# Performance work log

Measured on AMD Instinct MI355X. Metric: run time of the kernel, lower is better.

The kernel has to match this reference:

```python
import jax, jax.numpy as jnp
import numpy as np


def setup_inputs() -> dict:
    key = jax.random.key(0)
    ks = jax.random.split(key, 7)
    B, P, D = 4, 2048, 1024
    s = 1.0 / np.sqrt(D)
    return {
        "x":  jax.random.normal(ks[0], (B, P, D), dtype=jnp.float32),
        "Wq": jax.random.normal(ks[1], (D, D), dtype=jnp.float32) * s,
        "bq": jnp.zeros((D,), dtype=jnp.float32),
        "Wk": jax.random.normal(ks[2], (D, D), dtype=jnp.float32) * s,
        "bk": jnp.zeros((D,), dtype=jnp.float32),
        "Wv": jax.random.normal(ks[3], (D, D), dtype=jnp.float32) * s,
        "bv": jnp.zeros((D,), dtype=jnp.float32),
    }


def reference(x, Wq, bq, Wk, bk, Wv, bv):
    # x: [B, P, D]; Linear uses W stored torch-style [out, in]: y = x @ W.T + b
    b, p, d = x.shape
    q = jnp.einsum("bpd,ed->bpe", x, Wq) + bq
    k = jnp.einsum("bpd,ed->bpe", x, Wk) + bk
    v = jnp.einsum("bpd,ed->bpe", x, Wv) + bv
    attn = jnp.einsum("bqd,bkd->bqk", q, k)  # [B, P, P]
    causal = jnp.triu(jnp.ones((p, p), dtype=bool), k=1)  # True above diagonal
    attn = jnp.where(causal, -jnp.inf, attn)
    attn = attn / jnp.sqrt(jnp.asarray(d, dtype=attn.dtype))
    scores = jax.nn.softmax(attn, axis=-1)
    # dropout is identity in eval/deterministic mode
    return jnp.einsum("bqk,bkd->bqd", scores, v)
```

## Files before the change

### kernel.cpp

```cpp
#include <hip/hip_runtime.h>
#include <hip/hip_bf16.h>


typedef __attribute__((ext_vector_type(8))) short bf16x8;
typedef __attribute__((ext_vector_type(4))) float f32x4;

__device__ __forceinline__ unsigned short f2bf(float f) {
    union { float f; unsigned u; } v; v.f = f;
    unsigned r = v.u + 0x7FFF + ((v.u >> 16) & 1);
    return (unsigned short)(r >> 16);
}

__device__ __forceinline__ void gload_lds16(const unsigned short* g, unsigned short* l) {
    __builtin_amdgcn_global_load_lds(
        (const __attribute__((address_space(1))) unsigned int*)g,
        (__attribute__((address_space(3))) unsigned int*)l, 16, 0, 0);
}

__global__ void convert_kernel(const float* __restrict__ x,  const float* __restrict__ wq,
                               const float* __restrict__ wk, const float* __restrict__ wv,
                               const float* __restrict__ bq, const float* __restrict__ bk,
                               const float* __restrict__ bv,
                               unsigned short* __restrict__ xb, unsigned short* __restrict__ wqkvb,
                               float* __restrict__ bqkv, float* __restrict__ lsum) {
    long t = (long)blockIdx.x * blockDim.x + threadIdx.x;
    long idx = t * 4;
    const float* src; unsigned short* dst; long off;
    if      (idx <  8388608) { src = x;  dst = xb;            off = idx;            }
    else if (idx <  9437184) { src = wq; dst = wqkvb;         off = idx -  8388608; }
    else if (idx < 10485760) { src = wk; dst = wqkvb+1048576; off = idx -  9437184; }
    else if (idx < 11534336) { src = wv; dst = wqkvb+2097152; off = idx - 10485760; }
    else return;
    float4 v = *(const float4*)(src + off);
    ushort4 o = make_ushort4(f2bf(v.x), f2bf(v.y), f2bf(v.z), f2bf(v.w));
    *(ushort4*)(dst + off) = o;
    if (t < 768) {
        long o2 = t * 4;
        float4 b;
        if      (o2 < 1024) b = *(const float4*)(bq + o2);
        else if (o2 < 2048) b = *(const float4*)(bk + o2 - 1024);
        else                b = *(const float4*)(bv + o2 - 2048);
        *(float4*)(bqkv + o2) = b;
    }
    if (t >= 1024 && t < 3072) {
        float4 z = make_float4(0.f, 0.f, 0.f, 0.f);
        *(float4*)(lsum + (t - 1024) * 4) = z;
    }
}

__device__ __forceinline__ void stage(const unsigned short* gA, long lda,
                                      const unsigned short* gB, long ldb,
                                      unsigned short* As, unsigned short* Bs,
                                      int w, int k0) {
#pragma unroll
    for (int s = 0; s < 4; ++s) {
        gload_lds16(gA + k0 + (long)(s * 8) * lda, &As[(w * 32 + s * 8) * 64]);
        gload_lds16(gB + k0 + (long)(s * 8) * ldb, &Bs[(w * 32 + s * 8) * 64]);
    }
}

template<bool SWAP>
__device__ __forceinline__ void mfma_tile(const unsigned short* As, const unsigned short* Bs,
                                          int wr, int wc, int ln, int pr0, int pr1,
                                          f32x4 (&acc)[4][4]) {
#pragma unroll
    for (int kk = 0; kk < 2; ++kk) {
        const int pr = kk ? pr1 : pr0;
        bf16x8 af[4], bfr[4];
#pragma unroll
        for (int i = 0; i < 4; ++i)
            af[i] = *(const bf16x8*)(&As[(wr + i * 16 + ln) * 64 + pr]);
#pragma unroll
        for (int j = 0; j < 4; ++j)
            bfr[j] = *(const bf16x8*)(&Bs[(wc + j * 16 + ln) * 64 + pr]);
#pragma unroll
        for (int i = 0; i < 4; ++i)
#pragma unroll
            for (int j = 0; j < 4; ++j)
                acc[i][j] = SWAP
                    ? __builtin_amdgcn_mfma_f32_16x16x32_bf16(bfr[j], af[i], acc[i][j], 0, 0, 0)
                    : __builtin_amdgcn_mfma_f32_16x16x32_bf16(af[i], bfr[j], acc[i][j], 0, 0, 0);
    }
}

template<bool SWAP>
__device__ __forceinline__ void kloop_sb(const unsigned short* gA, long lda,
                                         const unsigned short* gB, long ldb,
                                         unsigned short* As, unsigned short* Bs,
                                         int w, int lane, int Keff, f32x4 (&acc)[4][4]) {
    const int q  = lane >> 4;
    const int ln = lane & 15;
    const int wr = (w >> 1) * 64;
    const int wc = (w & 1) * 64;
    const int pr0 = ((q)     ^ (ln & 7)) * 8;
    const int pr1 = ((q + 4) ^ (ln & 7)) * 8;
    for (int k0 = 0; k0 < Keff; k0 += 64) {
        stage(gA, lda, gB, ldb, As, Bs, w, k0);
        __syncthreads();
        mfma_tile<SWAP>(As, Bs, wr, wc, ln, pr0, pr1, acc);
        __syncthreads();
    }
}

template<bool SWAP>
__device__ __forceinline__ void kloop_db(const unsigned short* gA, long lda,
                                         const unsigned short* gB, long ldb,
                                         unsigned short* As0, unsigned short* Bs0,
                                         unsigned short* As1, unsigned short* Bs1,
                                         int w, int lane, int Keff, f32x4 (&acc)[4][4]) {
    const int q  = lane >> 4;
    const int ln = lane & 15;
    const int wr = (w >> 1) * 64;
    const int wc = (w & 1) * 64;
    const int pr0 = ((q)     ^ (ln & 7)) * 8;
    const int pr1 = ((q + 4) ^ (ln & 7)) * 8;
    stage(gA, lda, gB, ldb, As0, Bs0, w, 0);
    __syncthreads();
    for (int k0 = 0; k0 < Keff; k0 += 128) {
        stage(gA, lda, gB, ldb, As1, Bs1, w, k0 + 64);
        mfma_tile<SWAP>(As0, Bs0, wr, wc, ln, pr0, pr1, acc);
        __syncthreads();
        if (k0 + 128 < Keff)
            stage(gA, lda, gB, ldb, As0, Bs0, w, k0 + 128);
        mfma_tile<SWAP>(As1, Bs1, wr, wc, ln, pr0, pr1, acc);
        __syncthreads();
    }
}

__global__ __launch_bounds__(256, 3)
void gemm_qkv(const unsigned short* __restrict__ X,
              const unsigned short* __restrict__ W,
              unsigned short* __restrict__ QK,
              unsigned short* __restrict__ VT,
              const float* __restrict__ bias) {
    const int n0 = blockIdx.x * 128;
    const int m0 = blockIdx.y * 128;
    __shared__ __align__(16) unsigned short As0[128 * 64];
    __shared__ __align__(16) unsigned short Bs0[128 * 64 + 8192];
    const int tid = threadIdx.x, lane = tid & 63, w = tid >> 6;
    const int q = lane >> 4, ln = lane & 15;
    const int wr = (w >> 1) * 64, wc = (w & 1) * 64;
    const int srow = lane >> 3, sc = (lane & 7) ^ srow;
    const unsigned short* gA = X + (long)(m0 + w * 32 + srow) * 1024 + sc * 8;
    const unsigned short* gB = W + (long)(n0 + w * 32 + srow) * 1024 + sc * 8;
    f32x4 acc[4][4] = {};
    if (n0 >= 2048) {
        kloop_sb<false>(gA, 1024, gB, 1024, As0, Bs0, w, lane, 1024, acc);
#pragma unroll
        for (int j = 0; j < 4; ++j) {
            const int e = n0 - 2048 + wc + j * 16 + ln;
            const float bc = bias[n0 + wc + j * 16 + ln];
#pragma unroll
            for (int i = 0; i < 4; ++i) {
                const int m = m0 + wr + i * 16 + q * 4;
                ushort4 o = make_ushort4(f2bf(acc[i][j][0] + bc), f2bf(acc[i][j][1] + bc),
                                         f2bf(acc[i][j][2] + bc), f2bf(acc[i][j][3] + bc));
                *(ushort4*)(VT + (long)e * 8192 + m) = o;
            }
        }
    } else {
        kloop_sb<true>(gA, 1024, gB, 1024, As0, Bs0, w, lane, 1024, acc);
#pragma unroll
        for (int j = 0; j < 4; ++j) {
            const float4 bc = *(const float4*)(bias + n0 + wc + j * 16 + q * 4);
#pragma unroll
            for (int i = 0; i < 4; ++i) {
                const int m = m0 + wr + i * 16 + ln;
                const int n = n0 + wc + j * 16 + q * 4;
                ushort4 o = make_ushort4(f2bf(acc[i][j][0] + bc.x), f2bf(acc[i][j][1] + bc.y),
                                         f2bf(acc[i][j][2] + bc.z), f2bf(acc[i][j][3] + bc.w));
                *(ushort4*)(QK + (long)m * 2048 + n) = o;
            }
        }
    }
}

__device__ __forceinline__ void stage64(const unsigned short* gA, const unsigned short* gB,
                                        unsigned short* As, unsigned short* Bs,
                                        int w, int k0) {
    gload_lds16(gA + k0,                     &As[(w * 8) * 64]);
    gload_lds16(gA + k0 + (long)32 * 2048,   &As[(32 + w * 8) * 64]);
#pragma unroll
    for (int s = 0; s < 4; ++s)
        gload_lds16(gB + k0 + (long)(s * 32) * 2048, &Bs[(s * 32 + w * 8) * 64]);
}

__device__ __forceinline__ void mfma_tile64(const unsigned short* As, const unsigned short* Bs,
                                            int wr, int wc, int ln, int pr0, int pr1,
                                            f32x4 (&acc)[2][4]) {
#pragma unroll
    for (int kk = 0; kk < 2; ++kk) {
        const int pr = kk ? pr1 : pr0;
        bf16x8 af[2], bfr[4];
#pragma unroll
        for (int i = 0; i < 2; ++i)
            af[i] = *(const bf16x8*)(&As[(wr + i * 16 + ln) * 64 + pr]);
#pragma unroll
        for (int j = 0; j < 4; ++j)
            bfr[j] = *(const bf16x8*)(&Bs[(wc + j * 16 + ln) * 64 + pr]);
#pragma unroll
        for (int i = 0; i < 2; ++i)
#pragma unroll
            for (int j = 0; j < 4; ++j)
                acc[i][j] = __builtin_amdgcn_mfma_f32_16x16x32_bf16(bfr[j], af[i], acc[i][j], 0, 0, 0);
    }
}

__global__ __launch_bounds__(256, 3)
void gemm_scores(const unsigned short* __restrict__ QK,
                 unsigned short* __restrict__ P,
                 float* __restrict__ lsum) {
    const int t = blockIdx.x;
    int g = (int)((sqrtf(4.0f * t + 1.0f) - 1.0f) * 0.5f);
    while ((g + 1) * (g + 2) <= t) ++g;
    while (g * (g + 1) > t) --g;
    const int r  = t - g * (g + 1);
    const int gp = g + 1;
    const int i64 = 2 * g + (r >= gp ? 1 : 0);
    const int j   = (r >= gp) ? (r - gp) : r;
    const int m0 = i64 * 64, n0 = j * 128, z = blockIdx.y;
    const unsigned short* Qz = QK + (long)z * 2048 * 2048;
    const unsigned short* Kz = Qz + 1024;
    unsigned short* Pz = P + (long)z * 2048 * 2048;
    float* lz = lsum + z * 2048;

    __shared__ __align__(16) unsigned short As0[64 * 64], Bs0[128 * 64];
    __shared__ __align__(16) unsigned short As1[64 * 64], Bs1[128 * 64];
    const int tid = threadIdx.x, lane = tid & 63, w = tid >> 6;
    const int q = lane >> 4, ln = lane & 15;
    const int wr = (w >> 1) * 32, wc = (w & 1) * 64;
    const int srow = lane >> 3, sc = (lane & 7) ^ srow;
    const int pr0 = ((q)     ^ (ln & 7)) * 8;
    const int pr1 = ((q + 4) ^ (ln & 7)) * 8;
    const unsigned short* gA = Qz + (long)(m0 + w * 8 + srow) * 2048 + sc * 8;
    const unsigned short* gB = Kz + (long)(n0 + w * 8 + srow) * 2048 + sc * 8;
    f32x4 acc[2][4] = {};

    stage64(gA, gB, As0, Bs0, w, 0);
    __syncthreads();
    for (int k0 = 0; k0 < 1024; k0 += 128) {
        stage64(gA, gB, As1, Bs1, w, k0 + 64);
        mfma_tile64(As0, Bs0, wr, wc, ln, pr0, pr1, acc);
        __syncthreads();
        if (k0 + 128 < 1024)
            stage64(gA, gB, As0, Bs0, w, k0 + 128);
        mfma_tile64(As1, Bs1, wr, wc, ln, pr0, pr1, acc);
        __syncthreads();
    }

    const float scale = 0.03125f;
#pragma unroll
    for (int i2 = 0; i2 < 2; ++i2) {
        const int m = m0 + wr + i2 * 16 + ln;
        float rs = 0.f;
#pragma unroll
        for (int j2 = 0; j2 < 4; ++j2) {
            const int n = n0 + wc + j2 * 16 + q * 4;
            float p0 = (n     <= m) ? __expf(acc[i2][j2][0] * scale) : 0.f;
            float p1 = (n + 1 <= m) ? __expf(acc[i2][j2][1] * scale) : 0.f;
            float p2 = (n + 2 <= m) ? __expf(acc[i2][j2][2] * scale) : 0.f;
            float p3 = (n + 3 <= m) ? __expf(acc[i2][j2][3] * scale) : 0.f;
            rs += (p0 + p1) + (p2 + p3);
            ushort4 o = make_ushort4(f2bf(p0), f2bf(p1), f2bf(p2), f2bf(p3));
            *(ushort4*)(Pz + (long)m * 2048 + n) = o;
        }
        rs += __shfl_xor(rs, 16); rs += __shfl_xor(rs, 32);
        if (lane < 16) atomicAdd(&lz[m], rs);
    }
}

__global__ __launch_bounds__(256, 2)
void gemm_pv(const unsigned short* __restrict__ P,
             const unsigned short* __restrict__ VT,
             const float* __restrict__ lsum,
             float* __restrict__ out) {
    const int L  = blockIdx.x;
    const int ph = L >> 8;
    const int c  = L & 255;
    const int z  = c >> 6;
    const int r  = c & 63;
    const int mh = r >> 3;
    const int nt = r & 7;
    const int mt = ph ? 15 - mh : mh;
    const int m0 = mt * 128, n0 = nt * 128;
    const int Keff = m0 + 128;
    const unsigned short* Pz = P + (long)z * 2048 * 2048;
    const unsigned short* Vz = VT + (long)z * 2048;
    const float* lz = lsum + z * 2048;

    __shared__ __align__(16) unsigned short As0[128 * 64], Bs0[128 * 64];
    __shared__ __align__(16) unsigned short As1[128 * 64], Bs1[128 * 64];
    const int tid = threadIdx.x, lane = tid & 63, w = tid >> 6;
    const int q = lane >> 4, ln = lane & 15;
    const int wr = (w >> 1) * 64, wc = (w & 1) * 64;
    const int srow = lane >> 3, sc = (lane & 7) ^ srow;
    const unsigned short* gA = Pz + (long)(m0 + w * 32 + srow) * 2048 + sc * 8;
    const unsigned short* gB = Vz + (long)(n0 + w * 32 + srow) * 8192 + sc * 8;
    f32x4 acc[4][4] = {};
    kloop_db<true>(gA, 2048, gB, 8192, As0, Bs0, As1, Bs1, w, lane, Keff, acc);

#pragma unroll
    for (int i2 = 0; i2 < 4; ++i2) {
        const int m = m0 + wr + i2 * 16 + ln;
        const float inv = 1.0f / lz[m];
#pragma unroll
        for (int j2 = 0; j2 < 4; ++j2) {
            const int n = n0 + wc + j2 * 16 + q * 4;
            f32x4 o;
            o[0] = acc[i2][j2][0] * inv; o[1] = acc[i2][j2][1] * inv;
            o[2] = acc[i2][j2][2] * inv; o[3] = acc[i2][j2][3] * inv;
            __builtin_nontemporal_store(o, (f32x4*)(out + (long)(z * 2048 + m) * 1024 + n));
        }
    }
}

extern "C" void kernel_launch(void* const* d_in, const int* in_sizes, int n_in,
                              void* d_out, int out_size, void* d_ws, size_t ws_size,
                              hipStream_t stream) {
    const float* x  = (const float*)d_in[0];
    const float* Wq = (const float*)d_in[1];
    const float* bq = (const float*)d_in[2];
    const float* Wk = (const float*)d_in[3];
    const float* bk = (const float*)d_in[4];
    const float* Wv = (const float*)d_in[5];
    const float* bv = (const float*)d_in[6];
    float* out = (float*)d_out;

    char* ws = (char*)d_ws;
    unsigned short* xb    = (unsigned short*)ws; ws += (long)8192 * 1024 * 2;
    unsigned short* wqkvb = (unsigned short*)ws; ws += (long)3072 * 1024 * 2;
    float*          bqkv  = (float*)ws;          ws += (long)3072 * 4;
    float*          lsum  = (float*)ws;          ws += (long)8192 * 4;
    unsigned short* QKb   = (unsigned short*)ws; ws += (long)8192 * 2048 * 2;
    unsigned short* VTb   = (unsigned short*)ws; ws += (long)1024 * 8192 * 2;
    unsigned short* Pb    = (unsigned short*)ws; ws += (long)4 * 2048 * 2048 * 2;

    hipLaunchKernelGGL(convert_kernel, dim3(11264), dim3(256), 0, stream,
                       x, Wq, Wk, Wv, bq, bk, bv, xb, wqkvb, bqkv, lsum);

    hipLaunchKernelGGL(gemm_qkv, dim3(24, 64, 1), dim3(256), 0, stream,
                       xb, wqkvb, QKb, VTb, bqkv);

    hipLaunchKernelGGL(gemm_scores, dim3(272, 4, 1), dim3(256), 0, stream,
                       QKb, Pb, lsum);

    hipLaunchKernelGGL(gemm_pv, dim3(512, 1, 1), dim3(256), 0, stream,
                       Pb, VTb, lsum, out);
}
```

Before: 232.2 us.

## Use 64-row tiles with longest-first scheduling in PV GEMM

```diff
diff --git a/kernel.cpp b/kernel.cpp
--- a/kernel.cpp
+++ b/kernel.cpp
@@ -102,31 +102,6 @@
     }
 }
 
-template<bool SWAP>
-__device__ __forceinline__ void kloop_db(const unsigned short* gA, long lda,
-                                         const unsigned short* gB, long ldb,
-                                         unsigned short* As0, unsigned short* Bs0,
-                                         unsigned short* As1, unsigned short* Bs1,
-                                         int w, int lane, int Keff, f32x4 (&acc)[4][4]) {
-    const int q  = lane >> 4;
-    const int ln = lane & 15;
-    const int wr = (w >> 1) * 64;
-    const int wc = (w & 1) * 64;
-    const int pr0 = ((q)     ^ (ln & 7)) * 8;
-    const int pr1 = ((q + 4) ^ (ln & 7)) * 8;
-    stage(gA, lda, gB, ldb, As0, Bs0, w, 0);
-    __syncthreads();
-    for (int k0 = 0; k0 < Keff; k0 += 128) {
-        stage(gA, lda, gB, ldb, As1, Bs1, w, k0 + 64);
-        mfma_tile<SWAP>(As0, Bs0, wr, wc, ln, pr0, pr1, acc);
-        __syncthreads();
-        if (k0 + 128 < Keff)
-            stage(gA, lda, gB, ldb, As0, Bs0, w, k0 + 128);
-        mfma_tile<SWAP>(As1, Bs1, wr, wc, ln, pr0, pr1, acc);
-        __syncthreads();
-    }
-}
-
 __global__ __launch_bounds__(256, 3)
 void gemm_qkv(const unsigned short* __restrict__ X,
               const unsigned short* __restrict__ W,
@@ -175,14 +150,15 @@
     }
 }
 
-__device__ __forceinline__ void stage64(const unsigned short* gA, const unsigned short* gB,
+__device__ __forceinline__ void stage64(const unsigned short* gA, long lda,
+                                        const unsigned short* gB, long ldb,
                                         unsigned short* As, unsigned short* Bs,
                                         int w, int k0) {
-    gload_lds16(gA + k0,                     &As[(w * 8) * 64]);
-    gload_lds16(gA + k0 + (long)32 * 2048,   &As[(32 + w * 8) * 64]);
+    gload_lds16(gA + k0,                  &As[(w * 8) * 64]);
+    gload_lds16(gA + k0 + (long)32 * lda, &As[(32 + w * 8) * 64]);
 #pragma unroll
     for (int s = 0; s < 4; ++s)
-        gload_lds16(gB + k0 + (long)(s * 32) * 2048, &Bs[(s * 32 + w * 8) * 64]);
+        gload_lds16(gB + k0 + (long)(s * 32) * ldb, &Bs[(s * 32 + w * 8) * 64]);
 }
 
 __device__ __forceinline__ void mfma_tile64(const unsigned short* As, const unsigned short* Bs,
@@ -236,14 +212,14 @@
     const unsigned short* gB = Kz + (long)(n0 + w * 8 + srow) * 2048 + sc * 8;
     f32x4 acc[2][4] = {};
 
-    stage64(gA, gB, As0, Bs0, w, 0);
+    stage64(gA, 2048, gB, 2048, As0, Bs0, w, 0);
     __syncthreads();
     for (int k0 = 0; k0 < 1024; k0 += 128) {
-        stage64(gA, gB, As1, Bs1, w, k0 + 64);
+        stage64(gA, 2048, gB, 2048, As1, Bs1, w, k0 + 64);
         mfma_tile64(As0, Bs0, wr, wc, ln, pr0, pr1, acc);
         __syncthreads();
         if (k0 + 128 < 1024)
-            stage64(gA, gB, As0, Bs0, w, k0 + 128);
+            stage64(gA, 2048, gB, 2048, As0, Bs0, w, k0 + 128);
         mfma_tile64(As1, Bs1, wr, wc, ln, pr0, pr1, acc);
         __syncthreads();
     }
@@ -269,38 +245,48 @@
     }
 }
 
-__global__ __launch_bounds__(256, 2)
+__global__ __launch_bounds__(256, 3)
 void gemm_pv(const unsigned short* __restrict__ P,
              const unsigned short* __restrict__ VT,
              const float* __restrict__ lsum,
              float* __restrict__ out) {
-    const int L  = blockIdx.x;
-    const int ph = L >> 8;
-    const int c  = L & 255;
-    const int z  = c >> 6;
-    const int r  = c & 63;
-    const int mh = r >> 3;
-    const int nt = r & 7;
-    const int mt = ph ? 15 - mh : mh;
-    const int m0 = mt * 128, n0 = nt * 128;
-    const int Keff = m0 + 128;
+    const int L   = blockIdx.x;
+    const int z   = L & 3;
+    const int r   = L >> 2;
+    const int i64 = 31 - (r >> 3);
+    const int nt  = r & 7;
+    const int m0  = i64 * 64, n0 = nt * 128;
+    const int Keff = (i64 & 1) ? (m0 + 64) : (m0 + 128);
     const unsigned short* Pz = P + (long)z * 2048 * 2048;
     const unsigned short* Vz = VT + (long)z * 2048;
     const float* lz = lsum + z * 2048;
 
-    __shared__ __align__(16) unsigned short As0[128 * 64], Bs0[128 * 64];
-    __shared__ __align__(16) unsigned short As1[128 * 64], Bs1[128 * 64];
+    __shared__ __align__(16) unsigned short As0[64 * 64], Bs0[128 * 64];
+    __shared__ __align__(16) unsigned short As1[64 * 64], Bs1[128 * 64];
     const int tid = threadIdx.x, lane = tid & 63, w = tid >> 6;
     const int q = lane >> 4, ln = lane & 15;
-    const int wr = (w >> 1) * 64, wc = (w & 1) * 64;
+    const int wr = (w >> 1) * 32, wc = (w & 1) * 64;
     const int srow = lane >> 3, sc = (lane & 7) ^ srow;
-    const unsigned short* gA = Pz + (long)(m0 + w * 32 + srow) * 2048 + sc * 8;
-    const unsigned short* gB = Vz + (long)(n0 + w * 32 + srow) * 8192 + sc * 8;
-    f32x4 acc[4][4] = {};
-    kloop_db<true>(gA, 2048, gB, 8192, As0, Bs0, As1, Bs1, w, lane, Keff, acc);
-
-#pragma unroll
-    for (int i2 = 0; i2 < 4; ++i2) {
+    const int pr0 = ((q)     ^ (ln & 7)) * 8;
+    const int pr1 = ((q + 4) ^ (ln & 7)) * 8;
+    const unsigned short* gA = Pz + (long)(m0 + w * 8 + srow) * 2048 + sc * 8;
+    const unsigned short* gB = Vz + (long)(n0 + w * 8 + srow) * 8192 + sc * 8;
+    f32x4 acc[2][4] = {};
+
+    stage64(gA, 2048, gB, 8192, As0, Bs0, w, 0);
+    __syncthreads();
+    for (int k0 = 0; k0 < Keff; k0 += 128) {
+        stage64(gA, 2048, gB, 8192, As1, Bs1, w, k0 + 64);
+        mfma_tile64(As0, Bs0, wr, wc, ln, pr0, pr1, acc);
+        __syncthreads();
+        if (k0 + 128 < Keff)
+            stage64(gA, 2048, gB, 8192, As0, Bs0, w, k0 + 128);
+        mfma_tile64(As1, Bs1, wr, wc, ln, pr0, pr1, acc);
+        __syncthreads();
+    }
+
+#pragma unroll
+    for (int i2 = 0; i2 < 2; ++i2) {
         const int m = m0 + wr + i2 * 16 + ln;
         const float inv = 1.0f / lz[m];
 #pragma unroll
@@ -344,6 +330,6 @@
     hipLaunchKernelGGL(gemm_scores, dim3(272, 4, 1), dim3(256), 0, stream,
                        QKb, Pb, lsum);
 
-    hipLaunchKernelGGL(gemm_pv, dim3(512, 1, 1), dim3(256), 0, stream,
+    hipLaunchKernelGGL(gemm_pv, dim3(1024, 1, 1), dim3(256), 0, stream,
                        Pb, VTb, lsum, out);
 }
```

Result: faster. 220.0 us, median of 2 (-5.3%).
